# Kernel tuning notes

Measured on AMD Instinct MI355X. Metric: run time of the kernel, lower is better.

## Reference

```python
import jax, jax.numpy as jnp
import numpy as np

CUTOFF = 3.6
WIDTH = 0.3
N_MAX = 12
N_TYPES = 3
Y00 = 0.28209479177387814  # 1/sqrt(4*pi)
# GTO radial widths: sigma_n = cutoff * max(sqrt(n),1) / n_max
_SIGMA = np.array([CUTOFF * max(np.sqrt(n), 1.0) / N_MAX for n in range(N_MAX)], dtype=np.float32)
_NPOW = np.arange(N_MAX, dtype=np.float32)


def _cutoff_fn(r):
    # shifted cosine: 1 below cutoff-width, smooth cosine taper, 0 beyond cutoff
    start = CUTOFF - WIDTH
    taper = 0.5 * (1.0 + jnp.cos(jnp.pi * (r - start) / WIDTH))
    return jnp.where(r < start, 1.0, jnp.where(r < CUTOFF, taper, 0.0))


def _radial(r):
    # GTO-like basis: R_n(r) = r^n * exp(-r^2 / (2 sigma_n^2)), shape [E, N_MAX]
    r_ = r[:, None]
    return (r_ ** _NPOW) * jnp.exp(-0.5 * (r_ / _SIGMA) ** 2)


def _sph_harm(u):
    # real spherical harmonics up to l=2 on unit vectors u=[E,3] -> [E,9]
    x, y, z = u[:, 0], u[:, 1], u[:, 2]
    one = jnp.ones_like(x)
    return jnp.stack([
        0.28209479177387814 * one,                       # l=0
        0.4886025119029199 * y,                          # l=1, m=-1
        0.4886025119029199 * z,                          # l=1, m=0
        0.4886025119029199 * x,                          # l=1, m=+1
        1.0925484305920792 * x * y,                      # l=2, m=-2
        1.0925484305920792 * y * z,                      # l=2, m=-1
        0.31539156525252005 * (3.0 * z * z - 1.0),       # l=2, m=0
        1.0925484305920792 * x * z,                      # l=2, m=+1
        0.5462742152960396 * (x * x - y * y),            # l=2, m=+2
    ], axis=-1)


def _soap_energy(positions, weight, bias, atom_types, pairs):
    N = positions.shape[0]
    i, j = pairs[:, 0], pairs[:, 1]
    rij = positions[j] - positions[i]                     # [E,3] gather
    r = jnp.sqrt(jnp.sum(rij * rij, axis=-1) + 1e-12)     # [E]
    u = rij / r[:, None]
    # per-edge basis: [E, n, lm]
    B = _radial(r)[:, :, None] * _sph_harm(u)[:, None, :] * _cutoff_fn(r)[:, None, None]
    # scatter-sum by (center atom, neighbor species)
    seg = i.astype(jnp.int32) * N_TYPES + atom_types[j]
    c = jax.ops.segment_sum(B, seg, num_segments=N * N_TYPES)
    c = c.reshape(N, N_TYPES, N_MAX, 9)                    # [N, a, n, lm]
    # center-atom self density (r=0: only n=0, l=0 survives), weight 1.0
    c = c.at[jnp.arange(N), atom_types, 0, 0].add(Y00)
    # power spectrum per l block
    blocks = []
    for l, (lo, hi) in enumerate([(0, 1), (1, 4), (4, 9)]):
        cl = c[:, :, :, lo:hi]
        p = jnp.einsum('ianm,ibkm->ianbk', cl, cl) / jnp.sqrt(2.0 * l + 1.0)
        blocks.append(p)
    feats = jnp.stack(blocks, axis=-1).reshape(N, -1)      # [N, 3888]
    pooled = feats.sum(axis=0, keepdims=True)              # per_atom=False path
    return pooled @ weight.T + bias                        # [1, 1]


def setup_inputs() -> dict:
    key = jax.random.key(0)
    k1, k2, k3, k4 = jax.random.split(key, 4)
    N, E = 30000, 1000000
    positions = jax.random.normal(k1, (N, 3), dtype=jnp.float32) * 1.5
    atom_types = jax.random.randint(k2, (N,), 0, N_TYPES, dtype=jnp.int32)
    pairs = jax.random.randint(k3, (E, 2), 0, N, dtype=jnp.int32)
    weight = jax.random.normal(k4, (1, 3888), dtype=jnp.float32) * 0.01
    bias = jnp.zeros((1,), dtype=jnp.float32)
    return {"positions": positions, "weight": weight, "bias": bias,
            "atom_types": atom_types, "pairs": pairs}


def reference(positions, weight, bias, atom_types, pairs):
    return _soap_energy(positions, weight, bias, atom_types, pairs)
```

## Files before the change

kernel.cpp:

```cpp
#include <hip/hip_runtime.h>
#include <hip/hip_bf16.h>


#define NT 3
#define CPA 324
#define A_ELEMS 3888
#define BCAP 64
#define WPB 4

typedef __attribute__((ext_vector_type(4))) unsigned short ushort4v;
typedef unsigned long long ull;

#if __has_builtin(__builtin_amdgcn_exp2f)
__device__ __forceinline__ float exp2_fast(float x) { return __builtin_amdgcn_exp2f(x); }
#else
__device__ __forceinline__ float exp2_fast(float x) { return __expf(x * 0.6931471805599453f); }
#endif

__global__ void prep_kernel(const float* __restrict__ w,
                            const float* __restrict__ bias,
                            const float* __restrict__ pos,
                            const int* __restrict__ types,
                            float* __restrict__ A,
                            float4* __restrict__ posT,
                            int* __restrict__ cnt,
                            float* __restrict__ out, int N) {
    int t = blockIdx.x * blockDim.x + threadIdx.x;
    if (t == 0) out[0] = bias[0];
    if (t < A_ELEMS) {
        int l   = t / 1296;
        int rem = t - l * 1296;
        int an  = rem / 36;
        int bk  = rem - an * 36;
        int a = an / 12, n = an - (an / 12) * 12;
        int b = bk / 12, k = bk - (bk / 12) * 12;
        float inv = (l == 0) ? 1.0f : (l == 1 ? 0.57735026918962576f
                                              : 0.44721359549995794f);
        A[t] = w[a * 1296 + n * 108 + b * 36 + k * 3 + l] * inv;
    }
    if (t < N) {
        float4 p;
        p.x = pos[3 * t + 0];
        p.y = pos[3 * t + 1];
        p.z = pos[3 * t + 2];
        p.w = __int_as_float(types[t]);
        posT[t] = p;
        cnt[t] = 0;
    }
}

__global__ void build_kernel(const int* __restrict__ pairs,
                             const float4* __restrict__ posT,
                             int* __restrict__ cnt,
                             unsigned short* __restrict__ bucket, int E) {
    int t = blockIdx.x * blockDim.x + threadIdx.x;
    int e0 = t << 1;
    if (e0 >= E) return;
    int pi0, pj0, pi1 = 0, pj1 = 0;
    bool two = (e0 + 1) < E;
    if (two) {
        int4 p4 = ((const int4*)pairs)[t];
        pi0 = p4.x; pj0 = p4.y; pi1 = p4.z; pj1 = p4.w;
    } else {
        pi0 = pairs[2 * e0]; pj0 = pairs[2 * e0 + 1];
    }
    {
        float4 a = posT[pi0], b = posT[pj0];
        float dx = b.x - a.x, dy = b.y - a.y, dz = b.z - a.z;
        float r2 = dx * dx + dy * dy + dz * dz;
        if (r2 < 12.96f) {
            int p = atomicAdd(&cnt[pi0], 1);
            if (p < BCAP) bucket[(pi0 << 6) + p] = (unsigned short)pj0;
        }
    }
    if (two) {
        float4 a = posT[pi1], b = posT[pj1];
        float dx = b.x - a.x, dy = b.y - a.y, dz = b.z - a.z;
        float r2 = dx * dx + dy * dy + dz * dz;
        if (r2 < 12.96f) {
            int p = atomicAdd(&cnt[pi1], 1);
            if (p < BCAP) bucket[(pi1 << 6) + p] = (unsigned short)pj1;
        }
    }
}

__global__ void __launch_bounds__(256)
accum_kernel(const float4* __restrict__ posT,
             const int* __restrict__ cnt,
             const unsigned short* __restrict__ bucket,
             __hip_bfloat16* __restrict__ c2, int N) {
    __shared__ float sE[WPB][64][16];
    int wid = (blockIdx.x * blockDim.x + threadIdx.x) >> 6;
    int lane = threadIdx.x & 63;
    int wslot = (threadIdx.x >> 6);
    if (wid >= N) return;
    int i = wid;

    float4 pi = posT[i];
    int degv = cnt[i];
    degv = degv > BCAP ? BCAP : degv;
    int deg = __builtin_amdgcn_readfirstlane(degv);

    int jv = bucket[(i << 6) + lane];
    bool valid = lane < deg;
    int jsafe = valid ? jv : i;
    float4 pj = posT[jsafe];

    float dx = pj.x - pi.x, dy = pj.y - pi.y, dz = pj.z - pi.z;
    float u  = fmaf(dz, dz, fmaf(dy, dy, fmaf(dx, dx, 1e-12f)));
    float wv = __log2f(u);
    float lf = 0.0f;
    if (u >= 10.89f) {
        float r = sqrtf(u);
        float fcv = 0.5f + 0.5f * __cosf(10.471975511965978f * (r - 3.3f));
        lf = __log2f(fcv);
    }
    int tj = __float_as_int(pj.w);

    float t4 = dx * dy, t5 = dy * dz, t7 = dx * dz;
    float t6 = fmaf(dz, dz, -0.33333333333333333f * u);
    float t8 = fmaf(dx, dx, -(dy * dy));

    ull m0b = __ballot(valid && tj == 0);
    ull m1b = __ballot(valid && tj == 1);
    ull m2b = __ballot(valid && tj == 2);
    ull lt  = (lane == 63) ? 0x7FFFFFFFFFFFFFFFull : ((1ull << lane) - 1ull);
    int c0n = __popcll(m0b);
    int c1n = __popcll(m1b);
    int dest;
    if (!valid)          dest = deg + __popcll(~(m0b | m1b | m2b) & lt);
    else if (tj == 0)    dest = __popcll(m0b & lt);
    else if (tj == 1)    dest = c0n + __popcll(m1b & lt);
    else                 dest = c0n + c1n + __popcll(m2b & lt);

    float* rec = &sE[wslot][dest][0];
    ((float4*)rec)[0] = make_float4(u, wv, lf, 0.0f);
    ((float4*)rec)[1] = make_float4(1.0f, dy, dz, dx);
    ((float4*)rec)[2] = make_float4(t4, t5, t6, t7);
    ((float4*)rec)[3] = make_float4(t8, 0.0f, 0.0f, 0.0f);
    asm volatile("s_waitcnt lgkmcnt(0)" ::: "memory");

    int e1b = c0n + c1n;

    int n0 = lane % 12, m0 = lane / 12;
    int idx1 = lane + 64;
    bool has1 = idx1 < 108;
    int i1 = has1 ? idx1 : 0;
    int n1 = i1 % 12, m1 = i1 / 12;
    float fn0 = (float)n0, fn1 = (float)n1;
    float sg0 = 0.3f * fmaxf(sqrtf(fn0), 1.0f);
    float sg1 = 0.3f * fmaxf(sqrtf(fn1), 1.0f);
    float qc0 = -0.5f / (sg0 * sg0) * 1.4426950408889634f;
    float qc1 = -0.5f / (sg1 * sg1) * 1.4426950408889634f;
    int k0 = (m0 == 0) ? 0 : (m0 < 4 ? 1 : 2);
    int k1 = (m1 == 0) ? 0 : (m1 < 4 ? 1 : 2);
    float fnp0 = 0.5f * (fn0 - (float)k0);
    float fnp1 = 0.5f * (fn1 - (float)k1);

    const float* recb = &sE[wslot][0][0];
    const float* tp0 = recb + 4 + m0;
    const float* tp1 = recb + 4 + m1;

    float a00 = 0.f, a01 = 0.f, a02 = 0.f;
    float a10 = 0.f, a11 = 0.f, a12 = 0.f;

    #define EDGE_BODY(E_IDX, ACC0, ACC1)                                   \
    {                                                                      \
        int off = (E_IDX) << 4;                                            \
        float su  = recb[off + 0];                                         \
        float sw  = recb[off + 1];                                         \
        float slf = recb[off + 2];                                         \
        float tm0 = tp0[off];                                              \
        float tm1 = tp1[off];                                              \
        float rad0 = exp2_fast(fmaf(fnp0, sw, fmaf(qc0, su, slf)));        \
        float rad1 = exp2_fast(fmaf(fnp1, sw, fmaf(qc1, su, slf)));        \
        ACC0 = fmaf(rad0, tm0, ACC0);                                      \
        ACC1 = fmaf(rad1, tm1, ACC1);                                      \
    }

    int e = 0;
    #pragma unroll 2
    for (; e < c0n; ++e)  EDGE_BODY(e, a00, a10);
    #pragma unroll 2
    for (; e < e1b; ++e)  EDGE_BODY(e, a01, a11);
    #pragma unroll 2
    for (; e < deg; ++e)  EDGE_BODY(e, a02, a12);
    #undef EDGE_BODY

    __hip_bfloat16* cb = c2 + (size_t)i * CPA;
    cb[m0 * 36 + 0 * 12 + n0] = __float2bfloat16(a00);
    cb[m0 * 36 + 1 * 12 + n0] = __float2bfloat16(a01);
    cb[m0 * 36 + 2 * 12 + n0] = __float2bfloat16(a02);
    if (has1) {
        cb[m1 * 36 + 0 * 12 + n1] = __float2bfloat16(a10);
        cb[m1 * 36 + 1 * 12 + n1] = __float2bfloat16(a11);
        cb[m1 * 36 + 2 * 12 + n1] = __float2bfloat16(a12);
    }
}

__global__ void __launch_bounds__(576)
quad_kernel(const __hip_bfloat16* __restrict__ c2,
            const int* __restrict__ types,
            const float* __restrict__ A,
            float* __restrict__ out, int N) {
    __shared__ float sred[9];
    int m = __builtin_amdgcn_readfirstlane(threadIdx.x >> 6);
    int lane = threadIdx.x & 63;
    int i = blockIdx.x * 64 + lane;
    float dot = 0.0f;
    if (i < N) {
        float Km = m == 0 ? 0.28209479177387814f
                 : (m < 4 ? 0.4886025119029199f
                 : (m == 6 ? 0.94617469575756f
                 : (m == 8 ? 0.5462742152960396f : 1.0925484305920792f)));
        const ushort4v* cb4 =
            (const ushort4v*)(c2 + (size_t)i * CPA + m * 36);
        float v[36];
        #pragma unroll
        for (int q = 0; q < 9; ++q) {
            ushort4v u = cb4[q];
            #pragma unroll
            for (int r = 0; r < 4; ++r)
                v[q * 4 + r] = __uint_as_float(((unsigned)u[r]) << 16) * Km;
        }
        if (m == 0) {
            int ti = types[i];
            const float Y00 = 0.28209479177387814f;
            v[0]  += ti == 0 ? Y00 : 0.f;
            v[12] += ti == 1 ? Y00 : 0.f;
            v[24] += ti == 2 ? Y00 : 0.f;
        }
        int l = (m == 0) ? 0 : (m < 4 ? 1 : 2);
        const float* Al = A + l * 1296;
        #pragma unroll
        for (int an = 0; an < 36; ++an) {
            float s = 0.0f;
            #pragma unroll
            for (int b = 0; b < 36; ++b)
                s = fmaf(Al[an * 36 + b], v[b], s);
            dot = fmaf(v[an], s, dot);
        }
    }
    #pragma unroll
    for (int off = 32; off > 0; off >>= 1) dot += __shfl_down(dot, off, 64);
    if (lane == 0) sred[m] = dot;
    __syncthreads();
    if (threadIdx.x == 0) {
        float s = 0.f;
        #pragma unroll
        for (int kk = 0; kk < 9; ++kk) s += sred[kk];
        atomicAdd(out, s);
    }
}

extern "C" void kernel_launch(void* const* d_in, const int* in_sizes, int n_in,
                              void* d_out, int out_size, void* d_ws, size_t ws_size,
                              hipStream_t stream) {
    const float* pos   = (const float*)d_in[0];
    const float* w     = (const float*)d_in[1];
    const float* bias  = (const float*)d_in[2];
    const int*   types = (const int*)d_in[3];
    const int*   pairs = (const int*)d_in[4];
    float* out = (float*)d_out;

    int N = in_sizes[0] / 3;
    int E = in_sizes[4] / 2;

    char* ws = (char*)d_ws;
    size_t off = 0;
    float* A = (float*)(ws + off);             off += 16384;
    int* cnt = (int*)(ws + off);               off += ((size_t)N * 4 + 255) & ~(size_t)255;
    float4* posT = (float4*)(ws + off);        off += ((size_t)N * 16 + 255) & ~(size_t)255;
    unsigned short* bucket = (unsigned short*)(ws + off);
                                               off += ((size_t)N * BCAP * 2 + 255) & ~(size_t)255;
    __hip_bfloat16* c2 = (__hip_bfloat16*)(ws + off);

    int pblocks = (N + 255) / 256;
    prep_kernel<<<pblocks, 256, 0, stream>>>(w, bias, pos, types, A, posT, cnt, out, N);

    int ehalf = (E + 1) / 2;
    int eblocks = (ehalf + 255) / 256;
    build_kernel<<<eblocks, 256, 0, stream>>>(pairs, posT, cnt, bucket, E);

    int ablocks = ((size_t)N * 64 + 255) / 256;
    accum_kernel<<<ablocks, 256, 0, stream>>>(posT, cnt, bucket, c2, N);

    int qblocks = (N + 63) / 64;
    quad_kernel<<<qblocks, 576, 0, stream>>>(c2, types, A, out, N);
}
```

Before: 103.4 us.

## Precompute per-edge radial basis and normalized harmonics; widen build edges per thread

The accumulation kernel now has each lane (one per edge) compute the 12 radial exponentials once and store them with the unit-normalized angular terms in a padded shared-memory record (stride 25). The inner loop then does two LDS reads and an FMA per edge instead of evaluating exp2 for each (n, lm) output. Previously the exp folded in the r^-l normalization; it is now applied once per edge using rsqrt. The build kernel also handles four edges per thread with two int4 loads, so more gathers are in flight, and edge-loop unrolling goes from 2 to 4. The cost is more shared memory and registers per edge record.

Measured after the change: 94.67 us. 8.5% less time.

```diff
diff --git a/kernel.cpp b/kernel.cpp
--- a/kernel.cpp
+++ b/kernel.cpp
@@ -7,6 +7,7 @@
 #define A_ELEMS 3888
 #define BCAP 64
 #define WPB 4
+#define RSTRIDE 25
 
 typedef __attribute__((ext_vector_type(4))) unsigned short ushort4v;
 typedef unsigned long long ull;
@@ -49,37 +50,40 @@
     }
 }
 
+__device__ __forceinline__ void build_one(int i, int j,
+                                          const float4& a, const float4& b,
+                                          int* cnt, unsigned short* bucket) {
+    float dx = b.x - a.x, dy = b.y - a.y, dz = b.z - a.z;
+    float r2 = dx * dx + dy * dy + dz * dz;
+    if (r2 < 12.96f) {
+        int p = atomicAdd(&cnt[i], 1);
+        if (p < BCAP) bucket[(i << 6) + p] = (unsigned short)j;
+    }
+}
+
 __global__ void build_kernel(const int* __restrict__ pairs,
                              const float4* __restrict__ posT,
                              int* __restrict__ cnt,
                              unsigned short* __restrict__ bucket, int E) {
     int t = blockIdx.x * blockDim.x + threadIdx.x;
-    int e0 = t << 1;
+    int e0 = t << 2;
     if (e0 >= E) return;
-    int pi0, pj0, pi1 = 0, pj1 = 0;
-    bool two = (e0 + 1) < E;
-    if (two) {
-        int4 p4 = ((const int4*)pairs)[t];
-        pi0 = p4.x; pj0 = p4.y; pi1 = p4.z; pj1 = p4.w;
+    if (e0 + 4 <= E) {
+        int4 q0 = ((const int4*)pairs)[t * 2];
+        int4 q1 = ((const int4*)pairs)[t * 2 + 1];
+        float4 a0 = posT[q0.x], b0 = posT[q0.y];
+        float4 a1 = posT[q0.z], b1 = posT[q0.w];
+        float4 a2 = posT[q1.x], b2 = posT[q1.y];
+        float4 a3 = posT[q1.z], b3 = posT[q1.w];
+        build_one(q0.x, q0.y, a0, b0, cnt, bucket);
+        build_one(q0.z, q0.w, a1, b1, cnt, bucket);
+        build_one(q1.x, q1.y, a2, b2, cnt, bucket);
+        build_one(q1.z, q1.w, a3, b3, cnt, bucket);
     } else {
-        pi0 = pairs[2 * e0]; pj0 = pairs[2 * e0 + 1];
-    }
-    {
-        float4 a = posT[pi0], b = posT[pj0];
-        float dx = b.x - a.x, dy = b.y - a.y, dz = b.z - a.z;
-        float r2 = dx * dx + dy * dy + dz * dz;
-        if (r2 < 12.96f) {
-            int p = atomicAdd(&cnt[pi0], 1);
-            if (p < BCAP) bucket[(pi0 << 6) + p] = (unsigned short)pj0;
-        }
-    }
-    if (two) {
-        float4 a = posT[pi1], b = posT[pj1];
-        float dx = b.x - a.x, dy = b.y - a.y, dz = b.z - a.z;
-        float r2 = dx * dx + dy * dy + dz * dz;
-        if (r2 < 12.96f) {
-            int p = atomicAdd(&cnt[pi1], 1);
-            if (p < BCAP) bucket[(pi1 << 6) + p] = (unsigned short)pj1;
+        for (int e = e0; e < E; ++e) {
+            int i = pairs[2 * e], j = pairs[2 * e + 1];
+            float4 a = posT[i], b = posT[j];
+            build_one(i, j, a, b, cnt, bucket);
         }
     }
 }
@@ -89,7 +93,7 @@
              const int* __restrict__ cnt,
              const unsigned short* __restrict__ bucket,
              __hip_bfloat16* __restrict__ c2, int N) {
-    __shared__ float sE[WPB][64][16];
+    __shared__ float sE[WPB][64][RSTRIDE];
     int wid = (blockIdx.x * blockDim.x + threadIdx.x) >> 6;
     int lane = threadIdx.x & 63;
     int wslot = (threadIdx.x >> 6);
@@ -109,6 +113,8 @@
     float dx = pj.x - pi.x, dy = pj.y - pi.y, dz = pj.z - pi.z;
     float u  = fmaf(dz, dz, fmaf(dy, dy, fmaf(dx, dx, 1e-12f)));
     float wv = __log2f(u);
+    float ir = rsqrtf(u);
+    float iu = ir * ir;
     float lf = 0.0f;
     if (u >= 10.89f) {
         float r = sqrtf(u);
@@ -117,9 +123,15 @@
     }
     int tj = __float_as_int(pj.w);
 
-    float t4 = dx * dy, t5 = dy * dz, t7 = dx * dz;
-    float t6 = fmaf(dz, dz, -0.33333333333333333f * u);
-    float t8 = fmaf(dx, dx, -(dy * dy));
+    const float QC[12] = {
+        -8.014972449383130f, -8.014972449383130f, -4.007486224691565f,
+        -2.671657483127710f, -2.003743112345783f, -1.602994489876626f,
+        -1.335828741563855f, -1.144996064197590f, -1.001871556172891f,
+        -0.890552494375903f, -0.801497244938313f, -0.728633859034830f };
+    float R[12];
+    #pragma unroll
+    for (int n = 0; n < 12; ++n)
+        R[n] = exp2_fast(fmaf(0.5f * n, wv, fmaf(QC[n], u, lf)));
 
     ull m0b = __ballot(valid && tj == 0);
     ull m1b = __ballot(valid && tj == 1);
@@ -134,10 +146,15 @@
     else                 dest = c0n + c1n + __popcll(m2b & lt);
 
     float* rec = &sE[wslot][dest][0];
-    ((float4*)rec)[0] = make_float4(u, wv, lf, 0.0f);
-    ((float4*)rec)[1] = make_float4(1.0f, dy, dz, dx);
-    ((float4*)rec)[2] = make_float4(t4, t5, t6, t7);
-    ((float4*)rec)[3] = make_float4(t8, 0.0f, 0.0f, 0.0f);
+    #pragma unroll
+    for (int n = 0; n < 12; ++n) rec[n] = R[n];
+    rec[12] = 1.0f;
+    rec[13] = dy * ir;  rec[14] = dz * ir;  rec[15] = dx * ir;
+    rec[16] = dx * dy * iu;
+    rec[17] = dy * dz * iu;
+    rec[18] = fmaf(dz, dz, -0.33333333333333333f * u) * iu;
+    rec[19] = dx * dz * iu;
+    rec[20] = fmaf(dx, dx, -(dy * dy)) * iu;
     asm volatile("s_waitcnt lgkmcnt(0)" ::: "memory");
 
     int e1b = c0n + c1n;
@@ -147,43 +164,29 @@
     bool has1 = idx1 < 108;
     int i1 = has1 ? idx1 : 0;
     int n1 = i1 % 12, m1 = i1 / 12;
-    float fn0 = (float)n0, fn1 = (float)n1;
-    float sg0 = 0.3f * fmaxf(sqrtf(fn0), 1.0f);
-    float sg1 = 0.3f * fmaxf(sqrtf(fn1), 1.0f);
-    float qc0 = -0.5f / (sg0 * sg0) * 1.4426950408889634f;
-    float qc1 = -0.5f / (sg1 * sg1) * 1.4426950408889634f;
-    int k0 = (m0 == 0) ? 0 : (m0 < 4 ? 1 : 2);
-    int k1 = (m1 == 0) ? 0 : (m1 < 4 ? 1 : 2);
-    float fnp0 = 0.5f * (fn0 - (float)k0);
-    float fnp1 = 0.5f * (fn1 - (float)k1);
 
     const float* recb = &sE[wslot][0][0];
-    const float* tp0 = recb + 4 + m0;
-    const float* tp1 = recb + 4 + m1;
 
     float a00 = 0.f, a01 = 0.f, a02 = 0.f;
     float a10 = 0.f, a11 = 0.f, a12 = 0.f;
 
     #define EDGE_BODY(E_IDX, ACC0, ACC1)                                   \
     {                                                                      \
-        int off = (E_IDX) << 4;                                            \
-        float su  = recb[off + 0];                                         \
-        float sw  = recb[off + 1];                                         \
-        float slf = recb[off + 2];                                         \
-        float tm0 = tp0[off];                                              \
-        float tm1 = tp1[off];                                              \
-        float rad0 = exp2_fast(fmaf(fnp0, sw, fmaf(qc0, su, slf)));        \
-        float rad1 = exp2_fast(fmaf(fnp1, sw, fmaf(qc1, su, slf)));        \
-        ACC0 = fmaf(rad0, tm0, ACC0);                                      \
-        ACC1 = fmaf(rad1, tm1, ACC1);                                      \
+        const float* rp = recb + (E_IDX) * RSTRIDE;                        \
+        float Rv0 = rp[n0];                                                \
+        float Tv0 = rp[12 + m0];                                           \
+        float Rv1 = rp[n1];                                                \
+        float Tv1 = rp[12 + m1];                                           \
+        ACC0 = fmaf(Rv0, Tv0, ACC0);                                       \
+        ACC1 = fmaf(Rv1, Tv1, ACC1);                                       \
     }
 
     int e = 0;
-    #pragma unroll 2
+    #pragma unroll 4
     for (; e < c0n; ++e)  EDGE_BODY(e, a00, a10);
-    #pragma unroll 2
+    #pragma unroll 4
     for (; e < e1b; ++e)  EDGE_BODY(e, a01, a11);
-    #pragma unroll 2
+    #pragma unroll 4
     for (; e < deg; ++e)  EDGE_BODY(e, a02, a12);
     #undef EDGE_BODY
 
@@ -278,8 +281,8 @@
     int pblocks = (N + 255) / 256;
     prep_kernel<<<pblocks, 256, 0, stream>>>(w, bias, pos, types, A, posT, cnt, out, N);
 
-    int ehalf = (E + 1) / 2;
-    int eblocks = (ehalf + 255) / 256;
+    int equads = (E + 3) / 4;
+    int eblocks = (equads + 255) / 256;
     build_kernel<<<eblocks, 256, 0, stream>>>(pairs, posT, cnt, bucket, E);
 
     int ablocks = ((size_t)N * 64 + 255) / 256;
```
